# Optimization experiments

Hardware: AMD Instinct MI355X
Metric: run time of the kernel (lower is better)

The kernel has to match this reference:

```python
import jax, jax.numpy as jnp
import numpy as np

B, D, H = 524288, 128, 64  # batch, input_dim, hidden_dim; mask_dim = transform_dim = D//2 = 64


def _mlp(x, Wh, bh, Wo, bo):
    """eqx.nn.MLP with depth=3: 3 hidden relu layers then linear out.
    x: [B, in]; Wh: [3, H, in/H]; bh: [3, H]; Wo: [out, H]; bo: [out]."""
    h = x
    for i in range(Wh.shape[0]):  # fixed small layer loop
        h = jax.nn.relu(h @ Wh[i].T + bh[i])
    return h @ Wo.T + bo


def setup_inputs() -> dict:
    key = jax.random.key(0)
    ks = jax.random.split(key, 9)
    m = D // 2
    s = 1.0 / np.sqrt(H)  # lecun-ish init scale
    inp = {"x": jax.random.normal(ks[0], (B, D), dtype=jnp.float32)}
    inp["cond_Wh"] = jax.random.normal(ks[1], (3, H, m), dtype=jnp.float32) * s
    inp["cond_bh"] = jnp.zeros((3, H), dtype=jnp.float32)
    inp["cond_Wo"] = jax.random.normal(ks[2], (D - m, H), dtype=jnp.float32) * s
    inp["cond_bo"] = jnp.zeros((D - m,), dtype=jnp.float32)
    inp["scale_Wh"] = jax.random.normal(ks[3], (3, H, m), dtype=jnp.float32) * s
    inp["scale_bh"] = jnp.zeros((3, H), dtype=jnp.float32)
    inp["scale_Wo"] = jax.random.normal(ks[4], (D - m, H), dtype=jnp.float32) * s
    inp["scale_bo"] = jnp.zeros((D - m,), dtype=jnp.float32)
    return inp


def reference(x, cond_Wh, cond_bh, cond_Wo, cond_bo,
              scale_Wh, scale_bh, scale_Wo, scale_bo):
    m = x.shape[-1] // 2
    # mask = [1]*m + [0]*(D-m) -> mask_idx = [:m], transform_idx = [m:] (static contiguous split)
    x_masked = x[..., :m]
    x_transform = x[..., m:]
    shift = _mlp(x_masked, cond_Wh, cond_bh, cond_Wo, cond_bo)        # [B, D-m]
    log_scale = _mlp(x_masked, scale_Wh, scale_bh, scale_Wo, scale_bo)  # [B, D-m]
    scale = jnp.exp(jnp.clip(log_scale, -5, 3))
    y_transform = x_transform * scale + shift
    y = jnp.concatenate([x_masked, y_transform], axis=-1)  # scatter back (contiguous)
    logdet = jnp.sum(log_scale, axis=-1)  # note: unclipped log_scale, as in original
    return y, logdet
```

## Files before the change

kernel.cpp:

```cpp
#include <hip/hip_runtime.h>
#include <cstdint>

typedef __attribute__((ext_vector_type(8))) _Float16 half8;
typedef __attribute__((ext_vector_type(4))) _Float16 half4;
typedef __attribute__((ext_vector_type(4))) float f32x4;

__global__ void prep_weights(const float* __restrict__ cWh, const float* __restrict__ cWo,
                             const float* __restrict__ sWh, const float* __restrict__ sWo,
                             _Float16* __restrict__ wf) {
    int t = blockIdx.x * 256 + threadIdx.x;
    int e    = t & 7;
    int mt   = (t >> 3) & 3;
    int lane = (t >> 5) & 63;
    int kp   = (t >> 11) & 1;
    int L    = (t >> 12) & 7;
    const float* src = (L < 3)  ? cWh + L * 4096
                     : (L == 3) ? cWo
                     : (L < 7)  ? sWh + (L - 4) * 4096
                     :            sWo;
    int m = mt * 16 + (lane & 15);
    int k = (2 * kp + (e >> 2)) * 16 + 4 * (lane >> 4) + (e & 3);
    float w = src[m * 64 + k];
    _Float16 hi = (_Float16)w;
    _Float16 lo = (_Float16)(w - (float)hi);
    int off = lane * 32 + mt * 8 + e;
    int fi = (L * 2 + kp) * 2;
    wf[fi * 2048 + off]       = hi;
    wf[(fi + 1) * 2048 + off] = lo;
}

template<bool RELU>
__device__ __forceinline__ half8 cvt_frag(f32x4 a, f32x4 b) {
    half8 r;
#pragma unroll
    for (int i = 0; i < 4; ++i) {
        float va = RELU ? fmaxf(a[i], 0.f) : a[i];
        float vb = RELU ? fmaxf(b[i], 0.f) : b[i];
        r[i]     = (_Float16)va;
        r[i + 4] = (_Float16)vb;
    }
    return r;
}

__device__ __forceinline__ void run_layer(const _Float16* __restrict__ wf, int Lid,
                                          const float* __restrict__ bias, int lane, int g4,
                                          const half8 B[2][4], f32x4 acc[4][4]) {
#pragma unroll
    for (int mt = 0; mt < 4; ++mt) {
        f32x4 bb = *(const f32x4*)(bias + mt * 16 + g4);
#pragma unroll
        for (int nt = 0; nt < 4; ++nt) acc[mt][nt] = bb;
    }
#pragma unroll
    for (int kp = 0; kp < 2; ++kp) {
        half8 Ah[4], Al[4];
        const _Float16* p = wf + (Lid * 2 + kp) * 4096 + lane * 32;
#pragma unroll
        for (int mt = 0; mt < 4; ++mt) {
            Ah[mt] = *(const half8*)(p + mt * 8);
            Al[mt] = *(const half8*)(p + 2048 + mt * 8);
        }
#pragma unroll
        for (int nt = 0; nt < 4; ++nt)
#pragma unroll
            for (int mt = 0; mt < 4; ++mt) {
                acc[mt][nt] = __builtin_amdgcn_mfma_f32_16x16x32_f16(Ah[mt], B[kp][nt], acc[mt][nt], 0, 0, 0);
                acc[mt][nt] = __builtin_amdgcn_mfma_f32_16x16x32_f16(Al[mt], B[kp][nt], acc[mt][nt], 0, 0, 0);
            }
    }
}

__device__ __forceinline__ void acc_to_B_relu(const f32x4 acc[4][4], half8 B[2][4]) {
#pragma unroll
    for (int kp = 0; kp < 2; ++kp)
#pragma unroll
        for (int nt = 0; nt < 4; ++nt)
            B[kp][nt] = cvt_frag<true>(acc[2 * kp][nt], acc[2 * kp + 1][nt]);
}

__global__ __launch_bounds__(64, 2)
void coupling_main(const float* __restrict__ x,
                   const float* __restrict__ cbh, const float* __restrict__ cbo,
                   const float* __restrict__ sbh, const float* __restrict__ sbo,
                   const _Float16* __restrict__ wf,
                   float* __restrict__ y, float* __restrict__ logdet) {
    __shared__ float xstage[4096];
    const int lane = threadIdx.x;
    const int c = lane & 15;
    const int g = lane >> 4;
    const int g4 = g * 4;
    const long row0 = (long)blockIdx.x * 64;
    const float* xr = x + (row0 + c) * 128 + g4;
    float* yr = y + (row0 + c) * 128 + g4;

    f32x4 xm[4][4];
#pragma unroll
    for (int nt = 0; nt < 4; ++nt)
#pragma unroll
        for (int kt = 0; kt < 4; ++kt)
            xm[nt][kt] = *(const f32x4*)(xr + nt * 2048 + kt * 16);

    {
        const int rr = lane >> 4;
        const int s  = lane & 15;
#pragma unroll
        for (int i = 0; i < 16; ++i) {
            const int r = i * 4 + rr;
            const int j = s ^ (r & 7);
            const float* src = x + (row0 + r) * 128 + 64 + j * 4;
            __builtin_amdgcn_global_load_lds(
                (const __attribute__((address_space(1))) void*)src,
                (__attribute__((address_space(3))) void*)(xstage + i * 256),
                16, 0, 0);
        }
    }

    half8 B0[2][4];
#pragma unroll
    for (int nt = 0; nt < 4; ++nt) {
#pragma unroll
        for (int kt = 0; kt < 4; ++kt)
            *(f32x4*)(yr + nt * 2048 + kt * 16) = xm[nt][kt];
        B0[0][nt] = cvt_frag<false>(xm[nt][0], xm[nt][1]);
        B0[1][nt] = cvt_frag<false>(xm[nt][2], xm[nt][3]);
    }

    f32x4 acc[4][4];
    half8 B[2][4];

    run_layer(wf, 0, cbh,       lane, g4, B0, acc);
    acc_to_B_relu(acc, B);
    run_layer(wf, 1, cbh + 64,  lane, g4, B, acc);
    acc_to_B_relu(acc, B);
    run_layer(wf, 2, cbh + 128, lane, g4, B, acc);
    acc_to_B_relu(acc, B);
    run_layer(wf, 3, cbo,       lane, g4, B, acc);
    half4 shp[4][4];
#pragma unroll
    for (int mt = 0; mt < 4; ++mt)
#pragma unroll
        for (int nt = 0; nt < 4; ++nt) {
            half4 s;
#pragma unroll
            for (int i = 0; i < 4; ++i) s[i] = (_Float16)acc[mt][nt][i];
            shp[mt][nt] = s;
        }

    run_layer(wf, 4, sbh,       lane, g4, B0, acc);
    acc_to_B_relu(acc, B);
    run_layer(wf, 5, sbh + 64,  lane, g4, B, acc);
    acc_to_B_relu(acc, B);
    run_layer(wf, 6, sbh + 128, lane, g4, B, acc);
    acc_to_B_relu(acc, B);
    run_layer(wf, 7, sbo,       lane, g4, B, acc);

    asm volatile("s_waitcnt vmcnt(0)" ::: "memory");
    __builtin_amdgcn_sched_barrier(0);

    float pld0 = 0.f, pld1 = 0.f, pld2 = 0.f, pld3 = 0.f;
#pragma unroll
    for (int nt = 0; nt < 4; ++nt) {
        float psum = 0.f;
        const int r = nt * 16 + c;
#pragma unroll
        for (int mt = 0; mt < 4; ++mt) {
            f32x4 ls = acc[mt][nt];
            psum += ls[0] + ls[1] + ls[2] + ls[3];
            const int j = (mt * 4 + g) ^ (r & 7);
            f32x4 xt = *(const f32x4*)(xstage + r * 64 + j * 4);
            half4 sp = shp[mt][nt];
            f32x4 o;
#pragma unroll
            for (int i = 0; i < 4; ++i) {
                float cl = fminf(fmaxf(ls[i], -5.f), 3.f);
                o[i] = xt[i] * __expf(cl) + (float)sp[i];
            }
            *(f32x4*)(yr + nt * 2048 + 64 + mt * 16) = o;
        }
        if (nt == 0) pld0 = psum; else if (nt == 1) pld1 = psum;
        else if (nt == 2) pld2 = psum; else pld3 = psum;
    }
#pragma unroll
    for (int nt = 0; nt < 4; ++nt) {
        float v = (nt == 0) ? pld0 : (nt == 1) ? pld1 : (nt == 2) ? pld2 : pld3;
        v += __shfl_xor(v, 16);
        v += __shfl_xor(v, 32);
        if ((lane >> 4) == 0) logdet[row0 + nt * 16 + c] = v;
    }
}

extern "C" void kernel_launch(void* const* d_in, const int* in_sizes, int n_in,
                              void* d_out, int out_size, void* d_ws, size_t ws_size,
                              hipStream_t stream) {
    const float* x   = (const float*)d_in[0];
    const float* cWh = (const float*)d_in[1];
    const float* cbh = (const float*)d_in[2];
    const float* cWo = (const float*)d_in[3];
    const float* cbo = (const float*)d_in[4];
    const float* sWh = (const float*)d_in[5];
    const float* sbh = (const float*)d_in[6];
    const float* sWo = (const float*)d_in[7];
    const float* sbo = (const float*)d_in[8];

    const int B = in_sizes[0] / 128;

    _Float16* wf = (_Float16*)d_ws;

    prep_weights<<<128, 256, 0, stream>>>(cWh, cWo, sWh, sWo, wf);

    float* y = (float*)d_out;
    float* logdet = y + (size_t)B * 128;
    coupling_main<<<B / 64, 64, 0, stream>>>(x, cbh, cbo, sbh, sbo, wf, y, logdet);
}
```

Baseline: 167.5 us.

## Process two row tiles per block, prefetching second tile into LDS during compute

Each single-wave block now handles 128 rows instead of 64. The full second 64-row tile is loaded asynchronously into LDS while the first tile's MLPs run, which hides global load latency for the second tile. The grid is halved and LDS per block grows from 16 KB to 48 KB, which may lower occupancy. The second tile still runs its MLP compute serially after the first.

```diff
diff --git a/kernel.cpp b/kernel.cpp
--- a/kernel.cpp
+++ b/kernel.cpp
@@ -78,27 +78,96 @@
             B[kp][nt] = cvt_frag<true>(acc[2 * kp][nt], acc[2 * kp + 1][nt]);
 }
 
+__device__ __forceinline__ void run_mlps(const _Float16* __restrict__ wf,
+                                         const float* __restrict__ cbh, const float* __restrict__ cbo,
+                                         const float* __restrict__ sbh, const float* __restrict__ sbo,
+                                         int lane, int g4, const half8 B0[2][4],
+                                         half4 shp[4][4], f32x4 acc[4][4]) {
+    half8 B[2][4];
+    run_layer(wf, 0, cbh,       lane, g4, B0, acc);
+    acc_to_B_relu(acc, B);
+    run_layer(wf, 1, cbh + 64,  lane, g4, B, acc);
+    acc_to_B_relu(acc, B);
+    run_layer(wf, 2, cbh + 128, lane, g4, B, acc);
+    acc_to_B_relu(acc, B);
+    run_layer(wf, 3, cbo,       lane, g4, B, acc);
+#pragma unroll
+    for (int mt = 0; mt < 4; ++mt)
+#pragma unroll
+        for (int nt = 0; nt < 4; ++nt) {
+            half4 s;
+#pragma unroll
+            for (int i = 0; i < 4; ++i) s[i] = (_Float16)acc[mt][nt][i];
+            shp[mt][nt] = s;
+        }
+    run_layer(wf, 4, sbh,       lane, g4, B0, acc);
+    acc_to_B_relu(acc, B);
+    run_layer(wf, 5, sbh + 64,  lane, g4, B, acc);
+    acc_to_B_relu(acc, B);
+    run_layer(wf, 6, sbh + 128, lane, g4, B, acc);
+    acc_to_B_relu(acc, B);
+    run_layer(wf, 7, sbo,       lane, g4, B, acc);
+}
+
+__device__ __forceinline__ void epilogue(const f32x4 acc[4][4], const half4 shp[4][4],
+                                         const float* xts, int xstride, int xbase,
+                                         float* __restrict__ yr, float* __restrict__ logdet,
+                                         long row0, int lane, int c, int g) {
+    float pld0 = 0.f, pld1 = 0.f, pld2 = 0.f, pld3 = 0.f;
+#pragma unroll
+    for (int nt = 0; nt < 4; ++nt) {
+        float psum = 0.f;
+        const int r = nt * 16 + c;
+#pragma unroll
+        for (int mt = 0; mt < 4; ++mt) {
+            f32x4 ls = acc[mt][nt];
+            psum += ls[0] + ls[1] + ls[2] + ls[3];
+            const int j = xbase + (((mt * 4 + g) ^ (r & 7)) * 4);
+            f32x4 xt = *(const f32x4*)(xts + r * xstride + j);
+            half4 sp = shp[mt][nt];
+            f32x4 o;
+#pragma unroll
+            for (int i = 0; i < 4; ++i) {
+                float cl = fminf(fmaxf(ls[i], -5.f), 3.f);
+                o[i] = xt[i] * __expf(cl) + (float)sp[i];
+            }
+            *(f32x4*)(yr + nt * 2048 + 64 + mt * 16) = o;
+        }
+        if (nt == 0) pld0 = psum; else if (nt == 1) pld1 = psum;
+        else if (nt == 2) pld2 = psum; else pld3 = psum;
+    }
+#pragma unroll
+    for (int nt = 0; nt < 4; ++nt) {
+        float v = (nt == 0) ? pld0 : (nt == 1) ? pld1 : (nt == 2) ? pld2 : pld3;
+        v += __shfl_xor(v, 16);
+        v += __shfl_xor(v, 32);
+        if (g == 0) logdet[row0 + nt * 16 + c] = v;
+    }
+}
+
 __global__ __launch_bounds__(64, 2)
 void coupling_main(const float* __restrict__ x,
                    const float* __restrict__ cbh, const float* __restrict__ cbo,
                    const float* __restrict__ sbh, const float* __restrict__ sbo,
                    const _Float16* __restrict__ wf,
                    float* __restrict__ y, float* __restrict__ logdet) {
-    __shared__ float xstage[4096];
+    __shared__ float xstage0[4096];
+    __shared__ float xstage1[8192];
     const int lane = threadIdx.x;
     const int c = lane & 15;
     const int g = lane >> 4;
     const int g4 = g * 4;
-    const long row0 = (long)blockIdx.x * 64;
-    const float* xr = x + (row0 + c) * 128 + g4;
-    float* yr = y + (row0 + c) * 128 + g4;
-
+    const long row0 = (long)blockIdx.x * 128;
+    const long row1 = row0 + 64;
+
+    const float* xr0 = x + (row0 + c) * 128 + g4;
+    float* yr0 = y + (row0 + c) * 128 + g4;
     f32x4 xm[4][4];
 #pragma unroll
     for (int nt = 0; nt < 4; ++nt)
 #pragma unroll
         for (int kt = 0; kt < 4; ++kt)
-            xm[nt][kt] = *(const f32x4*)(xr + nt * 2048 + kt * 16);
+            xm[nt][kt] = *(const f32x4*)(xr0 + nt * 2048 + kt * 16);
 
     {
         const int rr = lane >> 4;
@@ -110,83 +179,62 @@
             const float* src = x + (row0 + r) * 128 + 64 + j * 4;
             __builtin_amdgcn_global_load_lds(
                 (const __attribute__((address_space(1))) void*)src,
-                (__attribute__((address_space(3))) void*)(xstage + i * 256),
+                (__attribute__((address_space(3))) void*)(xstage0 + i * 256),
                 16, 0, 0);
         }
     }
 
+    {
+        const int rr = lane >> 5;
+        const int s  = lane & 31;
+#pragma unroll
+        for (int i = 0; i < 32; ++i) {
+            const int r = i * 2 + rr;
+            const int j = s ^ (r & 7);
+            const float* src = x + (row1 + r) * 128 + j * 4;
+            __builtin_amdgcn_global_load_lds(
+                (const __attribute__((address_space(1))) void*)src,
+                (__attribute__((address_space(3))) void*)(xstage1 + i * 256),
+                16, 0, 0);
+        }
+    }
+
     half8 B0[2][4];
 #pragma unroll
     for (int nt = 0; nt < 4; ++nt) {
 #pragma unroll
         for (int kt = 0; kt < 4; ++kt)
-            *(f32x4*)(yr + nt * 2048 + kt * 16) = xm[nt][kt];
+            *(f32x4*)(yr0 + nt * 2048 + kt * 16) = xm[nt][kt];
         B0[0][nt] = cvt_frag<false>(xm[nt][0], xm[nt][1]);
         B0[1][nt] = cvt_frag<false>(xm[nt][2], xm[nt][3]);
     }
 
     f32x4 acc[4][4];
-    half8 B[2][4];
-
-    run_layer(wf, 0, cbh,       lane, g4, B0, acc);
-    acc_to_B_relu(acc, B);
-    run_layer(wf, 1, cbh + 64,  lane, g4, B, acc);
-    acc_to_B_relu(acc, B);
-    run_layer(wf, 2, cbh + 128, lane, g4, B, acc);
-    acc_to_B_relu(acc, B);
-    run_layer(wf, 3, cbo,       lane, g4, B, acc);
     half4 shp[4][4];
-#pragma unroll
-    for (int mt = 0; mt < 4; ++mt)
-#pragma unroll
-        for (int nt = 0; nt < 4; ++nt) {
-            half4 s;
-#pragma unroll
-            for (int i = 0; i < 4; ++i) s[i] = (_Float16)acc[mt][nt][i];
-            shp[mt][nt] = s;
-        }
-
-    run_layer(wf, 4, sbh,       lane, g4, B0, acc);
-    acc_to_B_relu(acc, B);
-    run_layer(wf, 5, sbh + 64,  lane, g4, B, acc);
-    acc_to_B_relu(acc, B);
-    run_layer(wf, 6, sbh + 128, lane, g4, B, acc);
-    acc_to_B_relu(acc, B);
-    run_layer(wf, 7, sbo,       lane, g4, B, acc);
+    run_mlps(wf, cbh, cbo, sbh, sbo, lane, g4, B0, shp, acc);
 
     asm volatile("s_waitcnt vmcnt(0)" ::: "memory");
     __builtin_amdgcn_sched_barrier(0);
-
-    float pld0 = 0.f, pld1 = 0.f, pld2 = 0.f, pld3 = 0.f;
-#pragma unroll
-    for (int nt = 0; nt < 4; ++nt) {
-        float psum = 0.f;
+    epilogue(acc, shp, xstage0, 64, 0, yr0, logdet, row0, lane, c, g);
+
+    float* yr1 = y + (row1 + c) * 128 + g4;
+#pragma unroll
+    for (int nt = 0; nt < 4; ++nt) {
         const int r = nt * 16 + c;
-#pragma unroll
-        for (int mt = 0; mt < 4; ++mt) {
-            f32x4 ls = acc[mt][nt];
-            psum += ls[0] + ls[1] + ls[2] + ls[3];
-            const int j = (mt * 4 + g) ^ (r & 7);
-            f32x4 xt = *(const f32x4*)(xstage + r * 64 + j * 4);
-            half4 sp = shp[mt][nt];
-            f32x4 o;
-#pragma unroll
-            for (int i = 0; i < 4; ++i) {
-                float cl = fminf(fmaxf(ls[i], -5.f), 3.f);
-                o[i] = xt[i] * __expf(cl) + (float)sp[i];
-            }
-            *(f32x4*)(yr + nt * 2048 + 64 + mt * 16) = o;
-        }
-        if (nt == 0) pld0 = psum; else if (nt == 1) pld1 = psum;
-        else if (nt == 2) pld2 = psum; else pld3 = psum;
-    }
-#pragma unroll
-    for (int nt = 0; nt < 4; ++nt) {
-        float v = (nt == 0) ? pld0 : (nt == 1) ? pld1 : (nt == 2) ? pld2 : pld3;
-        v += __shfl_xor(v, 16);
-        v += __shfl_xor(v, 32);
-        if ((lane >> 4) == 0) logdet[row0 + nt * 16 + c] = v;
-    }
+        f32x4 v[4];
+#pragma unroll
+        for (int kt = 0; kt < 4; ++kt) {
+            const int j = ((kt * 4 + g) ^ (r & 7)) * 4;
+            v[kt] = *(const f32x4*)(xstage1 + r * 128 + j);
+            *(f32x4*)(yr1 + nt * 2048 + kt * 16) = v[kt];
+        }
+        B0[0][nt] = cvt_frag<false>(v[0], v[1]);
+        B0[1][nt] = cvt_frag<false>(v[2], v[3]);
+    }
+
+    run_mlps(wf, cbh, cbo, sbh, sbo, lane, g4, B0, shp, acc);
+
+    epilogue(acc, shp, xstage1, 128, 64, yr1, logdet, row1, lane, c, g);
 }
 
 extern "C" void kernel_launch(void* const* d_in, const int* in_sizes, int n_in,
@@ -210,5 +258,5 @@
 
     float* y = (float*)d_out;
     float* logdet = y + (size_t)B * 128;
-    coupling_main<<<B / 64, 64, 0, stream>>>(x, cbh, cbo, sbh, sbo, wf, y, logdet);
-}
+    coupling_main<<<B / 128, 64, 0, stream>>>(x, cbh, cbo, sbh, sbo, wf, y, logdet);
+}
```

After: 235.9 us. +40.8%, slower.

## Stage full input rows in LDS and write output rows coalesced from LDS

Applied to the files above, without the earlier changes.

The whole 64x128 row tile is now loaded into LDS with async global-to-LDS loads, with staged vmcnt waits, instead of direct strided register loads for the masked half. The transformed results are written back into LDS and the full tile is then stored to global memory with contiguous per-row 16-byte stores. This targets strided 16-byte global access and aims for fully coalesced rows, at the cost of doubling LDS to 32KB, which may lower occupancy, and adding an LDS round trip. The vmcnt counts assume exactly 32 outstanding loads in order.

```diff
diff --git a/kernel.cpp b/kernel.cpp
--- a/kernel.cpp
+++ b/kernel.cpp
@@ -84,30 +84,21 @@
                    const float* __restrict__ sbh, const float* __restrict__ sbo,
                    const _Float16* __restrict__ wf,
                    float* __restrict__ y, float* __restrict__ logdet) {
-    __shared__ float xstage[4096];
+    __shared__ float xstage[8192];
     const int lane = threadIdx.x;
     const int c = lane & 15;
     const int g = lane >> 4;
     const int g4 = g * 4;
     const long row0 = (long)blockIdx.x * 64;
-    const float* xr = x + (row0 + c) * 128 + g4;
-    float* yr = y + (row0 + c) * 128 + g4;
-
-    f32x4 xm[4][4];
-#pragma unroll
-    for (int nt = 0; nt < 4; ++nt)
-#pragma unroll
-        for (int kt = 0; kt < 4; ++kt)
-            xm[nt][kt] = *(const f32x4*)(xr + nt * 2048 + kt * 16);
 
     {
-        const int rr = lane >> 4;
-        const int s  = lane & 15;
-#pragma unroll
-        for (int i = 0; i < 16; ++i) {
-            const int r = i * 4 + rr;
+        const int rr = lane >> 5;
+        const int s  = lane & 31;
+#pragma unroll
+        for (int i = 0; i < 32; ++i) {
+            const int r = i * 2 + rr;
             const int j = s ^ (r & 7);
-            const float* src = x + (row0 + r) * 128 + 64 + j * 4;
+            const float* src = x + (row0 + r) * 128 + j * 4;
             __builtin_amdgcn_global_load_lds(
                 (const __attribute__((address_space(1))) void*)src,
                 (__attribute__((address_space(3))) void*)(xstage + i * 256),
@@ -118,11 +109,24 @@
     half8 B0[2][4];
 #pragma unroll
     for (int nt = 0; nt < 4; ++nt) {
-#pragma unroll
-        for (int kt = 0; kt < 4; ++kt)
-            *(f32x4*)(yr + nt * 2048 + kt * 16) = xm[nt][kt];
-        B0[0][nt] = cvt_frag<false>(xm[nt][0], xm[nt][1]);
-        B0[1][nt] = cvt_frag<false>(xm[nt][2], xm[nt][3]);
+        if (nt == 0)      asm volatile("s_waitcnt vmcnt(24)" ::: "memory");
+        else if (nt == 1) asm volatile("s_waitcnt vmcnt(16)" ::: "memory");
+        else if (nt == 2) asm volatile("s_waitcnt vmcnt(8)"  ::: "memory");
+        else              asm volatile("s_waitcnt vmcnt(0)"  ::: "memory");
+        const int r = nt * 16 + c;
+        f32x4 v0, v1, v2, v3;
+        {
+            const int s0 = (0 * 4 + g) ^ (r & 7);
+            const int s1 = (1 * 4 + g) ^ (r & 7);
+            const int s2 = (2 * 4 + g) ^ (r & 7);
+            const int s3 = (3 * 4 + g) ^ (r & 7);
+            v0 = *(const f32x4*)(xstage + r * 128 + s0 * 4);
+            v1 = *(const f32x4*)(xstage + r * 128 + s1 * 4);
+            v2 = *(const f32x4*)(xstage + r * 128 + s2 * 4);
+            v3 = *(const f32x4*)(xstage + r * 128 + s3 * 4);
+        }
+        B0[0][nt] = cvt_frag<false>(v0, v1);
+        B0[1][nt] = cvt_frag<false>(v2, v3);
     }
 
     f32x4 acc[4][4];
@@ -153,9 +157,6 @@
     run_layer(wf, 6, sbh + 128, lane, g4, B, acc);
     acc_to_B_relu(acc, B);
     run_layer(wf, 7, sbo,       lane, g4, B, acc);
-
-    asm volatile("s_waitcnt vmcnt(0)" ::: "memory");
-    __builtin_amdgcn_sched_barrier(0);
 
     float pld0 = 0.f, pld1 = 0.f, pld2 = 0.f, pld3 = 0.f;
 #pragma unroll
@@ -166,8 +167,9 @@
         for (int mt = 0; mt < 4; ++mt) {
             f32x4 ls = acc[mt][nt];
             psum += ls[0] + ls[1] + ls[2] + ls[3];
-            const int j = (mt * 4 + g) ^ (r & 7);
-            f32x4 xt = *(const f32x4*)(xstage + r * 64 + j * 4);
+            const int slot = (16 + mt * 4 + g) ^ (r & 7);
+            float* p = xstage + r * 128 + slot * 4;
+            f32x4 xt = *(const f32x4*)p;
             half4 sp = shp[mt][nt];
             f32x4 o;
 #pragma unroll
@@ -175,7 +177,7 @@
                 float cl = fminf(fmaxf(ls[i], -5.f), 3.f);
                 o[i] = xt[i] * __expf(cl) + (float)sp[i];
             }
-            *(f32x4*)(yr + nt * 2048 + 64 + mt * 16) = o;
+            *(f32x4*)p = o;
         }
         if (nt == 0) pld0 = psum; else if (nt == 1) pld1 = psum;
         else if (nt == 2) pld2 = psum; else pld3 = psum;
@@ -186,6 +188,18 @@
         v += __shfl_xor(v, 16);
         v += __shfl_xor(v, 32);
         if ((lane >> 4) == 0) logdet[row0 + nt * 16 + c] = v;
+    }
+
+    {
+        const int rr = lane >> 5;
+        const int s  = lane & 31;
+#pragma unroll
+        for (int i = 0; i < 32; ++i) {
+            const int r = i * 2 + rr;
+            const int j = s ^ (r & 7);
+            f32x4 vv = *(const f32x4*)(xstage + i * 256 + lane * 4);
+            *(f32x4*)(y + (row0 + r) * 128 + j * 4) = vv;
+        }
     }
 }
 
```

After: 265.7 us. 58.6% more time.
